# Performance work log

Measured on AMD Instinct MI355X. Metric: run time of the kernel, lower is better.

The kernel has to match this reference:

```python
import jax, jax.numpy as jnp
import numpy as np

# Mamba block hyperparams (canonical: expand=2, d_state=16, d_conv=4, dt_rank=d_model/16)
D_MODEL = 1024
D_INNER = 2 * D_MODEL          # 2048
D_STATE = 16
D_CONV = 4
DT_RANK = D_MODEL // 16        # 64
B, L = 2, 1024


def setup_inputs() -> dict:
    key = jax.random.key(0)
    ks = jax.random.split(key, 12)
    s = lambda fan_in: 1.0 / np.sqrt(fan_in)
    x = jax.random.normal(ks[0], (B, L, D_MODEL), dtype=jnp.float32)
    W_in = jax.random.normal(ks[1], (D_MODEL, 2 * D_INNER), dtype=jnp.float32) * s(D_MODEL)
    conv_w = jax.random.normal(ks[2], (D_INNER, 1, D_CONV), dtype=jnp.float32) * s(D_CONV)
    conv_b = jax.random.normal(ks[3], (D_INNER,), dtype=jnp.float32) * 0.02
    W_xp = jax.random.normal(ks[4], (D_INNER, DT_RANK + 2 * D_STATE), dtype=jnp.float32) * s(D_INNER)
    W_dt = jax.random.normal(ks[5], (DT_RANK, D_INNER), dtype=jnp.float32) * s(DT_RANK)
    # dt bias init so softplus(dt_bias) ~ uniform in [1e-3, 1e-1] (mamba convention)
    dt = jnp.exp(jax.random.uniform(ks[6], (D_INNER,)) * (np.log(0.1) - np.log(1e-3)) + np.log(1e-3))
    dt_bias = dt + jnp.log(-jnp.expm1(-dt))  # inverse softplus
    A_log = jnp.log(jnp.broadcast_to(jnp.arange(1, D_STATE + 1, dtype=jnp.float32), (D_INNER, D_STATE)))
    D_skip = jnp.ones((D_INNER,), dtype=jnp.float32)
    W_out = jax.random.normal(ks[7], (D_INNER, D_MODEL), dtype=jnp.float32) * s(D_INNER)
    return {"x": x, "W_in": W_in, "conv_w": conv_w, "conv_b": conv_b, "W_xp": W_xp,
            "W_dt": W_dt, "dt_bias": dt_bias, "A_log": A_log, "D_skip": D_skip, "W_out": W_out}


def _causal_depthwise_conv(u, conv_w, conv_b):
    # u: [B, E, L], conv_w: [E, 1, K] depthwise, causal (left-pad K-1)
    K = conv_w.shape[-1]
    u = jnp.pad(u, ((0, 0), (0, 0), (K - 1, 0)))
    y = jax.lax.conv_general_dilated(
        u, conv_w, window_strides=(1,), padding='VALID',
        dimension_numbers=('NCH', 'OIH', 'NCH'), feature_group_count=u.shape[1])
    return y + conv_b[None, :, None]


def _selective_scan(u, delta, A, Bm, Cm, D_skip):
    # u, delta: [B,L,E]; A: [E,N]; Bm, Cm: [B,L,N]; D_skip: [E]
    dA = jnp.exp(jnp.einsum('ble,en->blen', delta, A))          # [B,L,E,N]
    dBu = jnp.einsum('ble,bln,ble->blen', delta, Bm, u)          # [B,L,E,N]

    def step(h, inp):
        dA_t, dBu_t, C_t = inp                                    # [B,E,N],[B,E,N],[B,N]
        h = dA_t * h + dBu_t
        y_t = jnp.einsum('ben,bn->be', h, C_t)
        return h, y_t

    h0 = jnp.zeros((u.shape[0], A.shape[0], A.shape[1]), dtype=u.dtype)
    xs = (jnp.swapaxes(dA, 0, 1), jnp.swapaxes(dBu, 0, 1), jnp.swapaxes(Cm, 0, 1))
    _, ys = jax.lax.scan(step, h0, xs)                            # ys: [L,B,E]
    y = jnp.swapaxes(ys, 0, 1)                                    # [B,L,E]
    return y + u * D_skip[None, None, :]


def reference(x, W_in, conv_w, conv_b, W_xp, W_dt, dt_bias, A_log, D_skip, W_out):
    # in_proj and gate split
    xz = x @ W_in                                                 # [B,L,2E]
    xp, z = jnp.split(xz, 2, axis=-1)                             # [B,L,E] each
    # causal depthwise conv + silu
    u = _causal_depthwise_conv(jnp.swapaxes(xp, 1, 2), conv_w, conv_b)
    u = jax.nn.silu(jnp.swapaxes(u, 1, 2))                        # [B,L,E]
    # input-dependent dt, B, C
    x_dbl = u @ W_xp                                              # [B,L,R+2N]
    dt_r, Bm, Cm = jnp.split(x_dbl, [DT_RANK, DT_RANK + D_STATE], axis=-1)
    delta = jax.nn.softplus(dt_r @ W_dt + dt_bias)                # [B,L,E]
    A = -jnp.exp(A_log)                                           # [E,N]
    y = _selective_scan(u, delta, A, Bm, Cm, D_skip)              # [B,L,E]
    # gate and out_proj
    y = y * jax.nn.silu(z)
    return y @ W_out                                              # [B,L,D]
```

## Files before the change

### kernel.cpp

```cpp
#include <hip/hip_runtime.h>
#include <math.h>

#define D_MODEL 1024
#define D_INNER 2048
#define D_STATE 16
#define D_CONV  4
#define DT_RANK 64
#define BB      2
#define LL      1024
#define BL      (BB*LL)
#define CHUNK   16
#define NCHUNK  (LL/CHUNK)
#define KSPLIT  16
#define KS_E    (D_INNER/KSPLIT)

typedef __attribute__((ext_vector_type(8))) short short8;
typedef __attribute__((ext_vector_type(4))) float f32x4;
typedef unsigned short ushort_t;
typedef unsigned int uint_t;

__device__ __forceinline__ float sigmoidf_(float x) { return 1.0f / (1.0f + __expf(-x)); }

__device__ __forceinline__ ushort_t f2bf(float f) {
    uint_t u = __float_as_uint(f);
    uint_t r = (u + 0x7fffu + ((u >> 16) & 1u)) >> 16;
    return (ushort_t)r;
}
__device__ __forceinline__ float bf2f(ushort_t v) {
    return __uint_as_float((uint_t)v << 16);
}

__device__ __forceinline__ void gload_lds16(const void* g, void* l) {
    __builtin_amdgcn_global_load_lds(
        (const __attribute__((address_space(1))) void*)g,
        (__attribute__((address_space(3))) void*)l,
        16, 0, 0);
}

template<int BM, int BN, int SPLIT, int BF0, int BF1>
__global__ __launch_bounds__(256)
void gemm_bf16_t(const ushort_t* __restrict__ A, const ushort_t* __restrict__ Bt,
                 void* __restrict__ C0v, void* __restrict__ C1v,
                 int M, int N, int K, int split) {
    constexpr int WMr = BM / 32;
    constexpr int WNr = BN / 32;
    const int nx = N / BN;
    const int nwg = nx * (M / BM);
    const int wg = ((blockIdx.x & 7) * (nwg >> 3)) + (blockIdx.x >> 3);
    const int row0 = (wg / nx) * BM;
    const int col0 = (wg % nx) * BN;

    __shared__ __align__(16) ushort_t As[BM * 32];
    __shared__ __align__(16) ushort_t Bs[BN * 32];

    const int tid  = threadIdx.x;
    const int lane = tid & 63;
    const int wave = tid >> 6;
    const int wr = wave >> 1, wc = wave & 1;

    f32x4 acc[WMr][WNr];
    #pragma unroll
    for (int m = 0; m < WMr; ++m)
        #pragma unroll
        for (int n = 0; n < WNr; ++n)
            acc[m][n] = (f32x4){0.f, 0.f, 0.f, 0.f};

    const ushort_t* Ablk = A  + (size_t)row0 * K;
    const ushort_t* Bblk = Bt + (size_t)col0 * K;
    const int r_ld  = tid >> 2;
    const int c8_ld = (tid & 3) * 8;

    for (int k0 = 0; k0 < K; k0 += 32) {
        #pragma unroll
        for (int i = 0; i < BM / 64; ++i)
            gload_lds16(Ablk + (size_t)(i * 64 + r_ld) * K + k0 + c8_ld,
                        &As[(i * 64 + wave * 16) * 32]);
        #pragma unroll
        for (int i = 0; i < BN / 64; ++i)
            gload_lds16(Bblk + (size_t)(i * 64 + r_ld) * K + k0 + c8_ld,
                        &Bs[(i * 64 + wave * 16) * 32]);
        __syncthreads();

        short8 af[WMr], bf[WNr];
        const int fr = lane & 15;
        const int kb = (lane >> 4) * 8;
        #pragma unroll
        for (int m = 0; m < WMr; ++m)
            af[m] = *(const short8*)&As[(wr * WMr * 16 + m * 16 + fr) * 32 + kb];
        #pragma unroll
        for (int n = 0; n < WNr; ++n)
            bf[n] = *(const short8*)&Bs[(wc * WNr * 16 + n * 16 + fr) * 32 + kb];

        #pragma unroll
        for (int m = 0; m < WMr; ++m)
            #pragma unroll
            for (int n = 0; n < WNr; ++n)
                acc[m][n] = __builtin_amdgcn_mfma_f32_16x16x32_bf16(
                    af[m], bf[n], acc[m][n], 0, 0, 0);
        __syncthreads();
    }

    const int crow = (lane >> 4) * 4;
    const int ccol = lane & 15;
    const bool second = SPLIT && (col0 >= split);
    const int ldc = second ? (N - split) : (SPLIT ? split : N);
    const int cb  = second ? (col0 - split) : col0;

    #pragma unroll
    for (int m = 0; m < WMr; ++m) {
        #pragma unroll
        for (int n = 0; n < WNr; ++n) {
            size_t base = (size_t)(row0 + wr * WMr * 16 + m * 16 + crow) * ldc
                          + cb + wc * WNr * 16 + n * 16 + ccol;
            if (second) {
                if (BF1) { ushort_t* cp = (ushort_t*)C1v + base;
                    #pragma unroll
                    for (int i = 0; i < 4; ++i) cp[(size_t)i * ldc] = f2bf(acc[m][n][i]);
                } else { float* cp = (float*)C1v + base;
                    #pragma unroll
                    for (int i = 0; i < 4; ++i) cp[(size_t)i * ldc] = acc[m][n][i];
                }
            } else {
                if (BF0) { ushort_t* cp = (ushort_t*)C0v + base;
                    #pragma unroll
                    for (int i = 0; i < 4; ++i) cp[(size_t)i * ldc] = f2bf(acc[m][n][i]);
                } else { float* cp = (float*)C0v + base;
                    #pragma unroll
                    for (int i = 0; i < 4; ++i) cp[(size_t)i * ldc] = acc[m][n][i];
                }
            }
        }
    }
}

__device__ __forceinline__ void transp_tile_body(const float* __restrict__ W,
                                                 ushort_t* __restrict__ Wt,
                                                 int R, int C, int bx, int by,
                                                 ushort_t (*tile)[33]) {
    int tx = threadIdx.x & 31, ty = threadIdx.x >> 5;
    int r0 = by * 32, c0 = bx * 32;
    #pragma unroll
    for (int i = 0; i < 32; i += 8)
        tile[ty + i][tx] = f2bf(W[(size_t)(r0 + ty + i) * C + c0 + tx]);
    __syncthreads();
    #pragma unroll
    for (int i = 0; i < 32; i += 8)
        Wt[(size_t)(c0 + ty + i) * R + r0 + tx] = tile[tx][ty + i];
}

__global__ __launch_bounds__(256)
void prep_kernel(const float* __restrict__ x, ushort_t* __restrict__ x_bf,
                 const float* __restrict__ W_in, ushort_t* __restrict__ Wint,
                 const float* __restrict__ W_out, ushort_t* __restrict__ Woutt) {
    __shared__ ushort_t tile[32][33];
    int bid = blockIdx.x;
    if (bid < 1024) {
        int i = (bid * 256 + threadIdx.x) * 8;
        float4 a = *reinterpret_cast<const float4*>(x + i);
        float4 b = *reinterpret_cast<const float4*>(x + i + 4);
        ushort_t o[8] = {f2bf(a.x), f2bf(a.y), f2bf(a.z), f2bf(a.w),
                         f2bf(b.x), f2bf(b.y), f2bf(b.z), f2bf(b.w)};
        *reinterpret_cast<short8*>(x_bf + i) = *reinterpret_cast<short8*>(o);
    } else if (bid < 1024 + 4096) {
        int bi = bid - 1024;
        transp_tile_body(W_in, Wint, 1024, 4096, bi & 127, bi >> 7, tile);
    } else {
        int bi = bid - 5120;
        transp_tile_body(W_out, Woutt, 2048, 1024, bi & 31, bi >> 5, tile);
    }
}

__global__ __launch_bounds__(256)
void gemm_xdbl_convfused(const ushort_t* __restrict__ xp, const float* __restrict__ W,
                         const float* __restrict__ conv_w, const float* __restrict__ conv_b,
                         float* __restrict__ part) {
    __shared__ float Ax[16][68];
    __shared__ float Au[16][65];
    __shared__ float Bs[16][96];

    const int tid = threadIdx.x;
    const int m0 = blockIdx.x * 64;
    const int kbase = blockIdx.y * KS_E;
    const int tx = tid & 15;
    const int ty = tid >> 4;
    const bool bhead = (m0 & (LL - 1)) == 0;

    float acc[4][6] = {};

    for (int k0 = 0; k0 < KS_E; k0 += 16) {
        for (int i = tid; i < 67 * 16; i += 256) {
            int r = i >> 4, k = i & 15;
            float v = 0.f;
            if (!(bhead && r < 3))
                v = bf2f(xp[(size_t)(m0 - 3 + r) * D_INNER + kbase + k0 + k]);
            Ax[k][r] = v;
        }
        #pragma unroll
        for (int j = 0; j < 6; ++j) {
            int idx = j * 256 + tid;
            int row = idx / 96, col = idx - row * 96;
            Bs[row][col] = W[(size_t)(kbase + k0 + row) * 96 + col];
        }
        __syncthreads();
        {
            float4 w4 = *(const float4*)&conv_w[(size_t)(kbase + k0 + tx) * 4];
            float cbv = conv_b[kbase + k0 + tx];
            #pragma unroll
            for (int rr = 0; rr < 4; ++rr) {
                int r = ty + rr * 16;
                float a = cbv;
                a = fmaf(w4.x, Ax[tx][r], a);
                a = fmaf(w4.y, Ax[tx][r + 1], a);
                a = fmaf(w4.z, Ax[tx][r + 2], a);
                a = fmaf(w4.w, Ax[tx][r + 3], a);
                Au[tx][r] = a * sigmoidf_(a);
            }
        }
        __syncthreads();
        #pragma unroll
        for (int kk = 0; kk < 16; ++kk) {
            float a[4], b[6];
            #pragma unroll
            for (int i = 0; i < 4; ++i) a[i] = Au[kk][ty * 4 + i];
            #pragma unroll
            for (int j = 0; j < 6; ++j) b[j] = Bs[kk][tx * 6 + j];
            #pragma unroll
            for (int i = 0; i < 4; ++i)
                #pragma unroll
                for (int j = 0; j < 6; ++j)
                    acc[i][j] = fmaf(a[i], b[j], acc[i][j]);
        }
        __syncthreads();
    }

    float* pblk = part + (size_t)blockIdx.y * BL * 96;
    #pragma unroll
    for (int i = 0; i < 4; ++i)
        #pragma unroll
        for (int j = 0; j < 6; ++j)
            pblk[(size_t)(m0 + ty * 4 + i) * 96 + tx * 6 + j] = acc[i][j];
}

__global__ __launch_bounds__(256)
void xdbl_reduce(const float* __restrict__ part, float* __restrict__ x_dbl) {
    int i = blockIdx.x * 256 + threadIdx.x;
    float s = 0.0f;
    #pragma unroll
    for (int k = 0; k < KSPLIT; ++k)
        s += part[(size_t)k * BL * 96 + i];
    x_dbl[i] = s;
}

template<int EPI>
__global__ __launch_bounds__(256)
void gemm_f32(const float* __restrict__ A, const float* __restrict__ B,
              float* __restrict__ C, const float* __restrict__ bias,
              int M, int N, int K, int lda, int ldb, int ldc) {
    __shared__ float As[16][65];
    __shared__ float Bs[16][64];

    const int tid = threadIdx.x;
    const int tx = tid & 15;
    const int ty = tid >> 4;
    const int row0 = blockIdx.y * 64;
    const int col0 = blockIdx.x * 64;

    const int arow = tid >> 4;
    const int acol = tid & 15;
    const int brow = tid >> 6;
    const int bcol = tid & 63;

    float acc[4][4] = {};

    for (int k0 = 0; k0 < K; k0 += 16) {
        #pragma unroll
        for (int p = 0; p < 4; ++p) {
            int r = arow + p * 16;
            As[acol][r] = A[(size_t)(row0 + r) * lda + (k0 + acol)];
        }
        int gc = col0 + bcol;
        #pragma unroll
        for (int p = 0; p < 4; ++p) {
            int r = brow + p * 4;
            Bs[r][bcol] = (gc < N) ? B[(size_t)(k0 + r) * ldb + gc] : 0.0f;
        }
        __syncthreads();
        #pragma unroll
        for (int kk = 0; kk < 16; ++kk) {
            float a[4];
            #pragma unroll
            for (int i = 0; i < 4; ++i) a[i] = As[kk][ty * 4 + i];
            float4 bv = *reinterpret_cast<const float4*>(&Bs[kk][tx * 4]);
            float b4[4] = {bv.x, bv.y, bv.z, bv.w};
            #pragma unroll
            for (int i = 0; i < 4; ++i)
                #pragma unroll
                for (int j = 0; j < 4; ++j)
                    acc[i][j] = fmaf(a[i], b4[j], acc[i][j]);
        }
        __syncthreads();
    }

    #pragma unroll
    for (int i = 0; i < 4; ++i) {
        int gr = row0 + ty * 4 + i;
        #pragma unroll
        for (int j = 0; j < 4; ++j) {
            int gc = col0 + tx * 4 + j;
            if (gc < N) {
                float v = acc[i][j];
                if (EPI == 1) {
                    v += bias[gc];
                    v = (v > 20.0f) ? v : log1pf(__expf(v));
                }
                C[(size_t)gr * ldc + gc] = v;
            }
        }
    }
}

__global__ __launch_bounds__(256)
void scan_phase1(const float* __restrict__ delta, const ushort_t* __restrict__ xp,
                 const float* __restrict__ conv_w, const float* __restrict__ conv_b,
                 const float* __restrict__ x_dbl, const float* __restrict__ A_log,
                 ushort_t* __restrict__ hend, float* __restrict__ sumdelta) {
    int g = blockIdx.x * 256 + threadIdx.x;
    int e = g & (D_INNER - 1);
    int c = (g >> 11) & (NCHUNK - 1);
    int b = g >> 17;

    float A_en[D_STATE];
    bool geo = true;
    #pragma unroll
    for (int n = 0; n < D_STATE; n += 4) {
        float4 al = *(const float4*)&A_log[e * D_STATE + n];
        A_en[n]     = -__expf(al.x);
        A_en[n + 1] = -__expf(al.y);
        A_en[n + 2] = -__expf(al.z);
        A_en[n + 3] = -__expf(al.w);
    }
    #pragma unroll
    for (int n = 0; n < D_STATE; ++n)
        geo = geo && (fabsf(A_en[n] + (float)(n + 1)) <= 2e-5f * (float)(n + 1));

    const int t0 = c * CHUNK;
    const float* dptr = delta + (size_t)(b * LL + t0) * D_INNER + e;
    const ushort_t* xptr = xp + (size_t)(b * LL + t0) * D_INNER + e;
    const float* xb   = x_dbl + (size_t)(b * LL + t0) * 96 + DT_RANK;
    float4 w4 = *(const float4*)&conv_w[(size_t)e * 4];
    float cbv = conv_b[e];

    float xw0 = 0.f, xw1 = 0.f, xw2 = 0.f;
    if (c > 0) {
        xw0 = bf2f(xptr[-3 * D_INNER]);
        xw1 = bf2f(xptr[-2 * D_INNER]);
        xw2 = bf2f(xptr[-1 * D_INNER]);
    }

    float h[D_STATE];
    #pragma unroll
    for (int n = 0; n < D_STATE; ++n) h[n] = 0.0f;
    float S = 0.0f;

    if (geo) {
        for (int t = 0; t < CHUNK; ++t) {
            float dv = dptr[(size_t)t * D_INNER];
            float x0 = bf2f(xptr[(size_t)t * D_INNER]);
            float a = cbv;
            a = fmaf(w4.x, xw0, a); a = fmaf(w4.y, xw1, a);
            a = fmaf(w4.z, xw2, a); a = fmaf(w4.w, x0, a);
            float uv = a * sigmoidf_(a);
            xw0 = xw1; xw1 = xw2; xw2 = x0;
            const float* xrow = xb + (size_t)t * 96;
            float4 B0 = *(const float4*)(xrow);
            float4 B1 = *(const float4*)(xrow + 4);
            float4 B2 = *(const float4*)(xrow + 8);
            float4 B3 = *(const float4*)(xrow + 12);
            float Bv[16] = {B0.x, B0.y, B0.z, B0.w, B1.x, B1.y, B1.z, B1.w,
                            B2.x, B2.y, B2.z, B2.w, B3.x, B3.y, B3.z, B3.w};
            S += dv;
            float du = dv * uv;
            float q = __expf(-dv);
            float dA = q;
            #pragma unroll
            for (int n = 0; n < D_STATE; ++n) {
                h[n] = fmaf(dA, h[n], du * Bv[n]);
                dA *= q;
            }
        }
    } else {
        for (int t = 0; t < CHUNK; ++t) {
            float dv = dptr[(size_t)t * D_INNER];
            float x0 = bf2f(xptr[(size_t)t * D_INNER]);
            float a = cbv;
            a = fmaf(w4.x, xw0, a); a = fmaf(w4.y, xw1, a);
            a = fmaf(w4.z, xw2, a); a = fmaf(w4.w, x0, a);
            float uv = a * sigmoidf_(a);
            xw0 = xw1; xw1 = xw2; xw2 = x0;
            const float* xrow = xb + (size_t)t * 96;
            float4 B0 = *(const float4*)(xrow);
            float4 B1 = *(const float4*)(xrow + 4);
            float4 B2 = *(const float4*)(xrow + 8);
            float4 B3 = *(const float4*)(xrow + 12);
            float Bv[16] = {B0.x, B0.y, B0.z, B0.w, B1.x, B1.y, B1.z, B1.w,
                            B2.x, B2.y, B2.z, B2.w, B3.x, B3.y, B3.z, B3.w};
            S += dv;
            float du = dv * uv;
            #pragma unroll
            for (int n = 0; n < D_STATE; ++n) {
                float dA = __expf(dv * A_en[n]);
                h[n] = fmaf(dA, h[n], du * Bv[n]);
            }
        }
    }

    size_t rbase = ((size_t)(c * BB + b) * D_STATE) * D_INNER + e;
    #pragma unroll
    for (int n = 0; n < D_STATE; ++n)
        hend[rbase + (size_t)n * D_INNER] = f2bf(h[n]);
    sumdelta[(size_t)(c * BB + b) * D_INNER + e] = S;
}

__global__ __launch_bounds__(256)
void scan_phase2(const float* __restrict__ A_log, const float* __restrict__ sumdelta,
                 ushort_t* __restrict__ hh) {
    int g = blockIdx.x * 256 + threadIdx.x;
    int e = g & (D_INNER - 1);
    int n = (g >> 11) & (D_STATE - 1);
    int b = g >> 15;
    float A_en = -__expf(A_log[e * D_STATE + n]);
    float np1 = (float)(n + 1);
    if (fabsf(A_en + np1) <= 2e-5f * np1) A_en = -np1;
    float h = 0.0f;
    for (int c = 0; c < NCHUNK; ++c) {
        size_t idx = ((size_t)(c * BB + b) * D_STATE + n) * D_INNER + e;
        float he = bf2f(hh[idx]);
        float dA = __expf(A_en * sumdelta[(size_t)(c * BB + b) * D_INNER + e]);
        hh[idx] = f2bf(h);
        h = fmaf(dA, h, he);
    }
}

__global__ __launch_bounds__(256)
void scan_phase3(const float* __restrict__ delta, const ushort_t* __restrict__ xp,
                 const float* __restrict__ conv_w, const float* __restrict__ conv_b,
                 const float* __restrict__ x_dbl, const ushort_t* __restrict__ zbf,
                 const float* __restrict__ A_log, const float* __restrict__ D_skip,
                 const ushort_t* __restrict__ hin, ushort_t* __restrict__ ybf) {
    int g = blockIdx.x * 256 + threadIdx.x;
    int e = g & (D_INNER - 1);
    int c = (g >> 11) & (NCHUNK - 1);
    int b = g >> 17;

    float A_en[D_STATE];
    bool geo = true;
    #pragma unroll
    for (int n = 0; n < D_STATE; n += 4) {
        float4 al = *(const float4*)&A_log[e * D_STATE + n];
        A_en[n]     = -__expf(al.x);
        A_en[n + 1] = -__expf(al.y);
        A_en[n + 2] = -__expf(al.z);
        A_en[n + 3] = -__expf(al.w);
    }
    #pragma unroll
    for (int n = 0; n < D_STATE; ++n)
        geo = geo && (fabsf(A_en[n] + (float)(n + 1)) <= 2e-5f * (float)(n + 1));

    float D_e = D_skip[e];
    float h[D_STATE];
    size_t rbase = ((size_t)(c * BB + b) * D_STATE) * D_INNER + e;
    #pragma unroll
    for (int n = 0; n < D_STATE; ++n)
        h[n] = bf2f(hin[rbase + (size_t)n * D_INNER]);

    const int t0 = c * CHUNK;
    const float* dptr = delta + (size_t)(b * LL + t0) * D_INNER + e;
    const ushort_t* xptr = xp + (size_t)(b * LL + t0) * D_INNER + e;
    const float* xb   = x_dbl + (size_t)(b * LL + t0) * 96 + DT_RANK;
    const ushort_t* zptr = zbf + (size_t)(b * LL + t0) * D_INNER + e;
    ushort_t* yout = ybf + (size_t)(b * LL + t0) * D_INNER + e;
    float4 w4 = *(const float4*)&conv_w[(size_t)e * 4];
    float cbv = conv_b[e];

    float xw0 = 0.f, xw1 = 0.f, xw2 = 0.f;
    if (c > 0) {
        xw0 = bf2f(xptr[-3 * D_INNER]);
        xw1 = bf2f(xptr[-2 * D_INNER]);
        xw2 = bf2f(xptr[-1 * D_INNER]);
    }

    if (geo) {
        for (int t = 0; t < CHUNK; ++t) {
            float dv = dptr[(size_t)t * D_INNER];
            float x0 = bf2f(xptr[(size_t)t * D_INNER]);
            float a = cbv;
            a = fmaf(w4.x, xw0, a); a = fmaf(w4.y, xw1, a);
            a = fmaf(w4.z, xw2, a); a = fmaf(w4.w, x0, a);
            float uv = a * sigmoidf_(a);
            xw0 = xw1; xw1 = xw2; xw2 = x0;
            const float* xrow = xb + (size_t)t * 96;
            float4 B0 = *(const float4*)(xrow);
            float4 B1 = *(const float4*)(xrow + 4);
            float4 B2 = *(const float4*)(xrow + 8);
            float4 B3 = *(const float4*)(xrow + 12);
            float4 C0 = *(const float4*)(xrow + 16);
            float4 C1 = *(const float4*)(xrow + 20);
            float4 C2 = *(const float4*)(xrow + 24);
            float4 C3 = *(const float4*)(xrow + 28);
            float Bv[16] = {B0.x, B0.y, B0.z, B0.w, B1.x, B1.y, B1.z, B1.w,
                            B2.x, B2.y, B2.z, B2.w, B3.x, B3.y, B3.z, B3.w};
            float Cv[16] = {C0.x, C0.y, C0.z, C0.w, C1.x, C1.y, C1.z, C1.w,
                            C2.x, C2.y, C2.z, C2.w, C3.x, C3.y, C3.z, C3.w};
            float du = dv * uv;
            float q = __expf(-dv);
            float dA = q;
            float y = 0.0f;
            #pragma unroll
            for (int n = 0; n < D_STATE; ++n) {
                h[n] = fmaf(dA, h[n], du * Bv[n]);
                y = fmaf(h[n], Cv[n], y);
                dA *= q;
            }
            float zv = bf2f(zptr[(size_t)t * D_INNER]);
            float yg = (y + uv * D_e) * (zv * sigmoidf_(zv));
            yout[(size_t)t * D_INNER] = f2bf(yg);
        }
    } else {
        for (int t = 0; t < CHUNK; ++t) {
            float dv = dptr[(size_t)t * D_INNER];
            float x0 = bf2f(xptr[(size_t)t * D_INNER]);
            float a = cbv;
            a = fmaf(w4.x, xw0, a); a = fmaf(w4.y, xw1, a);
            a = fmaf(w4.z, xw2, a); a = fmaf(w4.w, x0, a);
            float uv = a * sigmoidf_(a);
            xw0 = xw1; xw1 = xw2; xw2 = x0;
            const float* xrow = xb + (size_t)t * 96;
            float4 B0 = *(const float4*)(xrow);
            float4 B1 = *(const float4*)(xrow + 4);
            float4 B2 = *(const float4*)(xrow + 8);
            float4 B3 = *(const float4*)(xrow + 12);
            float4 C0 = *(const float4*)(xrow + 16);
            float4 C1 = *(const float4*)(xrow + 20);
            float4 C2 = *(const float4*)(xrow + 24);
            float4 C3 = *(const float4*)(xrow + 28);
            float Bv[16] = {B0.x, B0.y, B0.z, B0.w, B1.x, B1.y, B1.z, B1.w,
                            B2.x, B2.y, B2.z, B2.w, B3.x, B3.y, B3.z, B3.w};
            float Cv[16] = {C0.x, C0.y, C0.z, C0.w, C1.x, C1.y, C1.z, C1.w,
                            C2.x, C2.y, C2.z, C2.w, C3.x, C3.y, C3.z, C3.w};
            float du = dv * uv;
            float y = 0.0f;
            #pragma unroll
            for (int n = 0; n < D_STATE; ++n) {
                float dA = __expf(dv * A_en[n]);
                h[n] = fmaf(dA, h[n], du * Bv[n]);
                y = fmaf(h[n], Cv[n], y);
            }
            float zv = bf2f(zptr[(size_t)t * D_INNER]);
            float yg = (y + uv * D_e) * (zv * sigmoidf_(zv));
            yout[(size_t)t * D_INNER] = f2bf(yg);
        }
    }
}

extern "C" void kernel_launch(void* const* d_in, const int* in_sizes, int n_in,
                              void* d_out, int out_size, void* d_ws, size_t ws_size,
                              hipStream_t stream) {
    const float* x      = (const float*)d_in[0];
    const float* W_in   = (const float*)d_in[1];
    const float* conv_w = (const float*)d_in[2];
    const float* conv_b = (const float*)d_in[3];
    const float* W_xp   = (const float*)d_in[4];
    const float* W_dt   = (const float*)d_in[5];
    const float* dt_b   = (const float*)d_in[6];
    const float* A_log  = (const float*)d_in[7];
    const float* D_skip = (const float*)d_in[8];
    const float* W_out  = (const float*)d_in[9];
    float* out = (float*)d_out;

    const size_t M1 = 1024 * 1024;
    float* ws = (float*)d_ws;
    ushort_t* xp_bf = (ushort_t*)ws;
    ushort_t* hend  = (ushort_t*)(ws + 4 * M1);
    ushort_t* Wint_bf = (ushort_t*)(ws + 6 * M1);
    float*    delta = ws + 8 * M1;
    ushort_t* z_bf  = (ushort_t*)(ws + 12 * M1);
    float*    x_dbl = ws + 14 * M1;
    float*    sumd  = ws + 14 * M1 + 262144;
    ushort_t* ybf   = (ushort_t*)(ws + 14 * M1 + 524288);
    float*    xdbl_part = delta;
    ushort_t* x_bf  = ybf;
    ushort_t* Woutt_bf = (ushort_t*)(ws + 17 * M1);

    dim3 blk(256);

    hipLaunchKernelGGL(prep_kernel, dim3(1024 + 4096 + 2048), blk, 0, stream,
                       x, x_bf, W_in, Wint_bf, W_out, Woutt_bf);
    hipLaunchKernelGGL((gemm_bf16_t<64, 128, 1, 1, 1>),
                       dim3((BL / 64) * (4096 / 128)), blk, 0, stream,
                       x_bf, Wint_bf, (void*)xp_bf, (void*)z_bf,
                       BL, 2 * D_INNER, D_MODEL, D_INNER);
    hipLaunchKernelGGL(gemm_xdbl_convfused, dim3(BL / 64, KSPLIT), blk, 0, stream,
                       xp_bf, W_xp, conv_w, conv_b, xdbl_part);
    hipLaunchKernelGGL(xdbl_reduce, dim3((BL * 96) / 256), blk, 0, stream,
                       xdbl_part, x_dbl);
    hipLaunchKernelGGL((gemm_f32<1>), dim3(D_INNER / 64, BL / 64), blk, 0, stream,
                       x_dbl, W_dt, delta, dt_b, BL, D_INNER, DT_RANK, 96, D_INNER, D_INNER);
    hipLaunchKernelGGL(scan_phase1, dim3((BB * NCHUNK * D_INNER) / 256), blk, 0, stream,
                       delta, xp_bf, conv_w, conv_b, x_dbl, A_log, hend, sumd);
    hipLaunchKernelGGL(scan_phase2, dim3((BB * D_STATE * D_INNER) / 256), blk, 0, stream,
                       A_log, sumd, hend);
    hipLaunchKernelGGL(scan_phase3, dim3((BB * NCHUNK * D_INNER) / 256), blk, 0, stream,
                       delta, xp_bf, conv_w, conv_b, x_dbl, z_bf, A_log, D_skip, hend, ybf);
    hipLaunchKernelGGL((gemm_bf16_t<64, 64, 0, 0, 0>),
                       dim3((BL / 64) * (D_MODEL / 64)), blk, 0, stream,
                       ybf, Woutt_bf, (void*)out, (void*)out,
                       BL, D_MODEL, D_INNER, D_MODEL);
}
```

Before: 176.0 us.

## Split-K the out-projection GEMM and shrink in-proj tiles for more workgroups

```diff
diff --git a/kernel.cpp b/kernel.cpp
--- a/kernel.cpp
+++ b/kernel.cpp
@@ -37,18 +37,23 @@
         16, 0, 0);
 }
 
-template<int BM, int BN, int SPLIT, int BF0, int BF1>
-__global__ __launch_bounds__(256)
+template<int BM, int BN, int SPLIT, int BF0, int BF1, int KSPL>
+__global__ __launch_bounds__(256, 8)
 void gemm_bf16_t(const ushort_t* __restrict__ A, const ushort_t* __restrict__ Bt,
                  void* __restrict__ C0v, void* __restrict__ C1v,
                  int M, int N, int K, int split) {
     constexpr int WMr = BM / 32;
     constexpr int WNr = BN / 32;
     const int nx = N / BN;
-    const int nwg = nx * (M / BM);
+    const int per = nx * (M / BM);
+    const int nwg = per * KSPL;
     const int wg = ((blockIdx.x & 7) * (nwg >> 3)) + (blockIdx.x >> 3);
-    const int row0 = (wg / nx) * BM;
-    const int col0 = (wg % nx) * BN;
+    const int kz = (KSPL > 1) ? (wg / per) : 0;
+    const int rem = (KSPL > 1) ? (wg % per) : wg;
+    const int row0 = (rem / nx) * BM;
+    const int col0 = (rem % nx) * BN;
+    const int Kh = K / KSPL;
+    const int koff = kz * Kh;
 
     __shared__ __align__(16) ushort_t As[BM * 32];
     __shared__ __align__(16) ushort_t Bs[BN * 32];
@@ -65,12 +70,12 @@
         for (int n = 0; n < WNr; ++n)
             acc[m][n] = (f32x4){0.f, 0.f, 0.f, 0.f};
 
-    const ushort_t* Ablk = A  + (size_t)row0 * K;
-    const ushort_t* Bblk = Bt + (size_t)col0 * K;
+    const ushort_t* Ablk = A  + (size_t)row0 * K + koff;
+    const ushort_t* Bblk = Bt + (size_t)col0 * K + koff;
     const int r_ld  = tid >> 2;
     const int c8_ld = (tid & 3) * 8;
 
-    for (int k0 = 0; k0 < K; k0 += 32) {
+    for (int k0 = 0; k0 < Kh; k0 += 32) {
         #pragma unroll
         for (int i = 0; i < BM / 64; ++i)
             gload_lds16(Ablk + (size_t)(i * 64 + r_ld) * K + k0 + c8_ld,
@@ -102,6 +107,23 @@
 
     const int crow = (lane >> 4) * 4;
     const int ccol = lane & 15;
+
+    if (KSPL > 1) {
+        float* Cb = (float*)C0v + (size_t)kz * M * N;
+        #pragma unroll
+        for (int m = 0; m < WMr; ++m) {
+            #pragma unroll
+            for (int n = 0; n < WNr; ++n) {
+                float* cp = Cb + (size_t)(row0 + wr * WMr * 16 + m * 16 + crow) * N
+                               + col0 + wc * WNr * 16 + n * 16 + ccol;
+                #pragma unroll
+                for (int i = 0; i < 4; ++i)
+                    cp[(size_t)i * N] = acc[m][n][i];
+            }
+        }
+        return;
+    }
+
     const bool second = SPLIT && (col0 >= split);
     const int ldc = second ? (N - split) : (SPLIT ? split : N);
     const int cb  = second ? (col0 - split) : col0;
@@ -130,6 +152,17 @@
                 }
             }
         }
+    }
+}
+
+__global__ __launch_bounds__(256)
+void out_reduce(const float* __restrict__ part, float* __restrict__ out, int n) {
+    int i = (blockIdx.x * 256 + threadIdx.x) * 4;
+    if (i + 4 <= n) {
+        float4 a = *reinterpret_cast<const float4*>(part + i);
+        float4 b = *reinterpret_cast<const float4*>(part + n + i);
+        float4 r = {a.x + b.x, a.y + b.y, a.z + b.z, a.w + b.w};
+        *reinterpret_cast<float4*>(out + i) = r;
     }
 }
 
@@ -588,6 +621,7 @@
     float*    sumd  = ws + 14 * M1 + 262144;
     ushort_t* ybf   = (ushort_t*)(ws + 14 * M1 + 524288);
     float*    xdbl_part = delta;
+    float*    out_part  = delta;
     ushort_t* x_bf  = ybf;
     ushort_t* Woutt_bf = (ushort_t*)(ws + 17 * M1);
 
@@ -595,8 +629,8 @@
 
     hipLaunchKernelGGL(prep_kernel, dim3(1024 + 4096 + 2048), blk, 0, stream,
                        x, x_bf, W_in, Wint_bf, W_out, Woutt_bf);
-    hipLaunchKernelGGL((gemm_bf16_t<64, 128, 1, 1, 1>),
-                       dim3((BL / 64) * (4096 / 128)), blk, 0, stream,
+    hipLaunchKernelGGL((gemm_bf16_t<64, 64, 1, 1, 1, 1>),
+                       dim3((BL / 64) * (4096 / 64)), blk, 0, stream,
                        x_bf, Wint_bf, (void*)xp_bf, (void*)z_bf,
                        BL, 2 * D_INNER, D_MODEL, D_INNER);
     hipLaunchKernelGGL(gemm_xdbl_convfused, dim3(BL / 64, KSPLIT), blk, 0, stream,
@@ -611,8 +645,10 @@
                        A_log, sumd, hend);
     hipLaunchKernelGGL(scan_phase3, dim3((BB * NCHUNK * D_INNER) / 256), blk, 0, stream,
                        delta, xp_bf, conv_w, conv_b, x_dbl, z_bf, A_log, D_skip, hend, ybf);
-    hipLaunchKernelGGL((gemm_bf16_t<64, 64, 0, 0, 0>),
-                       dim3((BL / 64) * (D_MODEL / 64)), blk, 0, stream,
-                       ybf, Woutt_bf, (void*)out, (void*)out,
+    hipLaunchKernelGGL((gemm_bf16_t<64, 64, 0, 0, 0, 2>),
+                       dim3((BL / 64) * (D_MODEL / 64) * 2), blk, 0, stream,
+                       ybf, Woutt_bf, (void*)out_part, (void*)out_part,
                        BL, D_MODEL, D_INNER, D_MODEL);
-}
+    hipLaunchKernelGGL(out_reduce, dim3((BL * D_MODEL) / (256 * 4)), blk, 0, stream,
+                       out_part, out, BL * D_MODEL);
+}
```

After: 181.7 us. 3.2% more time.
